# Performance work log

Hardware: AMD Instinct MI355X
Metric: run time of the kernel (lower is better)

## Reference

```python
import jax, jax.numpy as jnp
import numpy as np

B, N, H = 1024, 200, 64


def setup_inputs() -> dict:
    key = jax.random.key(0)
    ks = jax.random.split(key, 8)
    A = jax.random.uniform(ks[0], (B, 2 * N, N), dtype=jnp.float32)
    hidden = jax.random.normal(ks[1], (B, N, H), dtype=jnp.float32)
    s = 1.0 / np.sqrt(H)
    w_ih = jax.random.normal(ks[2], (3 * H, 2 * H), dtype=jnp.float32) * s
    w_hh = jax.random.normal(ks[3], (3 * H, H), dtype=jnp.float32) * s
    b_ih = jnp.zeros((3 * H,), jnp.float32)
    b_hh = jnp.zeros((3 * H,), jnp.float32)
    b_iah = jnp.zeros((H,), jnp.float32)
    b_oah = jnp.zeros((H,), jnp.float32)
    W_in = jax.random.normal(ks[4], (H, H), dtype=jnp.float32) * s
    bias_in = jnp.zeros((H,), jnp.float32)
    W_out = jax.random.normal(ks[5], (H, H), dtype=jnp.float32) * s
    bias_out = jnp.zeros((H,), jnp.float32)
    return {"A": A, "hidden": hidden, "w_ih": w_ih, "w_hh": w_hh,
            "b_ih": b_ih, "b_hh": b_hh, "b_iah": b_iah, "b_oah": b_oah,
            "W_in": W_in, "bias_in": bias_in, "W_out": W_out, "bias_out": bias_out}


def reference(A, hidden, w_ih, w_hh, b_ih, b_hh, b_iah, b_oah,
              W_in, bias_in, W_out, bias_out):
    # SessionGNN._cell, step=1.
    n = A.shape[1] // 2
    A_in, A_out = A[:, :n, :], A[:, n:, :]          # (B, N, N) each
    h_in = jnp.einsum('bnh,gh->bng', hidden, W_in) + bias_in    # (B, N, H)
    h_out = jnp.einsum('bnh,gh->bng', hidden, W_out) + bias_out
    input_in = jnp.matmul(A_in, h_in) + b_iah       # (B, N, H)
    input_out = jnp.matmul(A_out, h_out) + b_oah
    inputs = jnp.concatenate([input_in, input_out], axis=2)     # (B, N, 2H)
    gi = jnp.einsum('bni,gi->bng', inputs, w_ih) + b_ih         # (B, N, 3H)
    gh = jnp.einsum('bnh,gh->bng', hidden, w_hh) + b_hh
    i_r, i_i, i_n = jnp.split(gi, 3, axis=2)
    h_r, h_i, h_n = jnp.split(gh, 3, axis=2)
    resetgate = jax.nn.sigmoid(i_r + h_r)
    inputgate = jax.nn.sigmoid(i_i + h_i)
    newgate = jnp.tanh(i_n + resetgate * h_n)
    return hidden - inputgate * (hidden - newgate)
```

## Files before the change

kernel.cpp:

```cpp
#include <hip/hip_runtime.h>

typedef _Float16 f16;
typedef __attribute__((ext_vector_type(4))) _Float16 f16x4;
typedef __attribute__((ext_vector_type(8))) _Float16 f16x8;
typedef __attribute__((ext_vector_type(4))) float f32x4;

#define MFMA16(a, b, c) __builtin_amdgcn_mfma_f32_16x16x32_f16((a), (b), (c), 0, 0, 0)

__device__ __forceinline__ f16x8 cvt8(float4 a, float4 b) {
    f16x8 r;
    r[0] = (f16)a.x; r[1] = (f16)a.y; r[2] = (f16)a.z; r[3] = (f16)a.w;
    r[4] = (f16)b.x; r[5] = (f16)b.y; r[6] = (f16)b.z; r[7] = (f16)b.w;
    return r;
}

__device__ __forceinline__ f16x8 zero8() {
    f16x8 z;
#pragma unroll
    for (int q = 0; q < 8; ++q) z[q] = (f16)0.0f;
    return z;
}

__global__ void prep_kernel(const float* __restrict__ w_ih, const float* __restrict__ w_hh,
                            const float* __restrict__ b_ih, const float* __restrict__ b_hh,
                            const float* __restrict__ b_iah, const float* __restrict__ b_oah,
                            const float* __restrict__ W_in, const float* __restrict__ bias_in,
                            const float* __restrict__ W_out, const float* __restrict__ bias_out,
                            f16* __restrict__ Wc, f16* __restrict__ Whh, f16* __restrict__ Wih,
                            float* __restrict__ cstA, float* __restrict__ cstB,
                            float* __restrict__ biasc) {
    const int gid = blockIdx.x * 256 + threadIdx.x;
    const int gstride = gridDim.x * 256;
    for (int i = gid; i < 8192; i += gstride)
        Wc[i] = (f16)(i < 4096 ? W_in[i] : W_out[i - 4096]);
    for (int i = gid; i < 12288; i += gstride) Whh[i] = (f16)w_hh[i];
    for (int i = gid; i < 24576; i += gstride) Wih[i] = (f16)w_ih[i];
    for (int job = gid; job < 768; job += gstride) {
        const int g = job >> 2, q = job & 3;
        float s = (q == 0) ? b_ih[g] : 0.0f;
        const float* wr = w_ih + g * 128 + q * 32;
        for (int i = 0; i < 32; ++i)
            s += wr[i] * ((q * 32 + i < 64) ? b_iah[q * 32 + i] : b_oah[q * 32 + i - 64]);
        atomicAdd(&cstA[g], s);
    }
    for (int g = gid; g < 192; g += gstride) cstB[g] = b_hh[g];
    for (int j = gid; j < 128; j += gstride) biasc[j] = (j < 64) ? bias_in[j] : bias_out[j - 64];
}

__global__ void zero_kernel(float* __restrict__ cstA) {
    if (threadIdx.x < 192) cstA[threadIdx.x] = 0.0f;
}

__global__ __launch_bounds__(512, 2) void gru_fused(
    const float* __restrict__ A, const float* __restrict__ hidden,
    const f16* __restrict__ Wc, const f16* __restrict__ Whh, const f16* __restrict__ Wih,
    const float* __restrict__ cstA, const float* __restrict__ cstB,
    const float* __restrict__ biasc, float* __restrict__ out) {
    extern __shared__ __align__(16) char lds_raw[];
    f16* hT  = (f16*)lds_raw;
    f16* hA  = (f16*)(lds_raw + 51200);
    f16* inp = (f16*)lds_raw;

    const int b = blockIdx.x;
    const float* Ab = A + (size_t)b * 80000;
    const float* hb = hidden + (size_t)b * 12800;
    float* ob = out + (size_t)b * 12800;

    const int tid = threadIdx.x;
    const int w   = tid >> 6;
    const int l   = tid & 63;
    const int l15 = l & 15;
    const int lg  = l >> 4;

    for (int mt = w; mt < 13; mt += 8) {
        const int m  = mt * 16 + l15;
        const int mc = m < 200 ? m : 199;
        const float* hrow = hb + mc * 64;
        float4 r0 = *(const float4*)(hrow + lg * 8);
        float4 r1 = *(const float4*)(hrow + lg * 8 + 4);
        float4 r2 = *(const float4*)(hrow + 32 + lg * 8);
        float4 r3 = *(const float4*)(hrow + 32 + lg * 8 + 4);
        f16x8 a0 = cvt8(r0, r1), a1 = cvt8(r2, r3);
        const int m0 = mt * 16 + lg * 4;
#pragma unroll
        for (int jt = 0; jt < 8; ++jt) {
            const int j = jt * 16 + l15;
            f32x4 acc = {0.f, 0.f, 0.f, 0.f};
            acc = MFMA16(a0, *(const f16x8*)(Wc + j * 64 + lg * 8), acc);
            acc = MFMA16(a1, *(const f16x8*)(Wc + j * 64 + 32 + lg * 8), acc);
            const float bc = biasc[j];
            if (m0 < 200) {
                f16x4 pk;
                pk[0] = (f16)(acc[0] + bc); pk[1] = (f16)(acc[1] + bc);
                pk[2] = (f16)(acc[2] + bc); pk[3] = (f16)(acc[3] + bc);
                *(f16x4*)(hT + j * 200 + m0) = pk;
            }
        }
    }
    __syncthreads();

    const int hf = w >> 2;
    const f16* hTp = hT + (w * 16 + l15) * 200;

    int s_h[4], s_row[4], s_unit[4]; bool s_act[4];
#pragma unroll
    for (int r = 0; r < 4; ++r) {
        const int idx = tid + r * 512;
        s_act[r] = idx < 1600;
        const int ic = s_act[r] ? idx : 0;
        s_h[r] = ic / 800;
        const int rem = ic % 800;
        s_row[r] = rem / 50; s_unit[r] = rem % 50;
    }

#define P2_LOADS(T, V)                                                            \
    {                                                                             \
        _Pragma("unroll")                                                         \
        for (int r = 0; r < 4; ++r) if (s_act[r]) {                               \
            const int n = (T) * 16 + s_row[r];                                    \
            const int nc = n < 200 ? n : 199;                                     \
            V[r] = *(const float4*)(Ab + (size_t)(s_h[r] * 200 + nc) * 200        \
                                    + s_unit[r] * 4);                             \
        }                                                                         \
    }
#define P2_WRITE(BUF, V)                                                          \
    {                                                                             \
        _Pragma("unroll")                                                         \
        for (int r = 0; r < 4; ++r) if (s_act[r]) {                               \
            const int idx = tid + r * 512;                                        \
            f16x4 pk;                                                             \
            pk[0] = (f16)V[r].x; pk[1] = (f16)V[r].y;                             \
            pk[2] = (f16)V[r].z; pk[3] = (f16)V[r].w;                             \
            *(f16x4*)(hA + (BUF) * 6400 + idx * 4) = pk;                          \
        }                                                                         \
    }

    f32x4 accC[13];
#pragma unroll
    for (int t = 0; t < 13; ++t) accC[t] = (f32x4){0.f, 0.f, 0.f, 0.f};

    float4 vA[4], vB[4];
    P2_LOADS(0, vA);
    P2_WRITE(0, vA);
    P2_LOADS(1, vB);
    __syncthreads();

#pragma unroll
    for (int t = 0; t < 13; ++t) {
        if (t + 2 <= 12) {
            if ((t & 1) == 0) { P2_LOADS(t + 2, vA); }
            else              { P2_LOADS(t + 2, vB); }
        }
        {
            const f16* hAp = hA + (t & 1) * 6400 + hf * 3200 + l15 * 200;
#pragma unroll
            for (int k0 = 0; k0 < 224; k0 += 32) {
                const int koff = (k0 == 192) ? 192 : k0 + lg * 8;
                f16x8 a;
                if (k0 == 192 && lg != 0) a = zero8();
                else                      a = *(const f16x8*)(hAp + koff);
                f16x8 bf = *(const f16x8*)(hTp + koff);
                accC[t] = MFMA16(a, bf, accC[t]);
            }
        }
        if (t + 1 <= 12) {
            if (((t + 1) & 1) == 0) { P2_WRITE(0, vA); }
            else                    { P2_WRITE(1, vB); }
        }
        __syncthreads();
    }
#undef P2_LOADS
#undef P2_WRITE

#pragma unroll
    for (int t = 0; t < 13; ++t) {
#pragma unroll
        for (int r = 0; r < 4; ++r) {
            const int n = t * 16 + lg * 4 + r;
            if (n < 200) inp[n * 136 + w * 16 + l15] = (f16)accC[t][r];
        }
    }
    __syncthreads();

    const int c   = w & 3;
    const int wm2 = w >> 2;
    const int hcol = c * 16 + l15;
    f16x8 Wf0[4], Wf1[4], Wf2[4];
#pragma unroll
    for (int k = 0; k < 4; ++k) {
        Wf0[k] = *(const f16x8*)(Wih + (hcol      ) * 128 + k * 32 + lg * 8);
        Wf1[k] = *(const f16x8*)(Wih + (64  + hcol) * 128 + k * 32 + lg * 8);
        Wf2[k] = *(const f16x8*)(Wih + (128 + hcol) * 128 + k * 32 + lg * 8);
    }
    f16x8 Hf0[2], Hf1[2], Hf2[2];
#pragma unroll
    for (int k = 0; k < 2; ++k) {
        Hf0[k] = *(const f16x8*)(Whh + (hcol      ) * 64 + k * 32 + lg * 8);
        Hf1[k] = *(const f16x8*)(Whh + (64  + hcol) * 64 + k * 32 + lg * 8);
        Hf2[k] = *(const f16x8*)(Whh + (128 + hcol) * 64 + k * 32 + lg * 8);
    }
    const float cAr = cstA[hcol], cAi = cstA[64 + hcol], cAn = cstA[128 + hcol];
    const float cBr = cstB[hcol], cBi = cstB[64 + hcol], cBn = cstB[128 + hcol];

    for (int t = wm2; t < 13; t += 2) {
        const int n  = t * 16 + l15;
        const int nc = n < 200 ? n : 199;
        f32x4 gir = {0.f,0.f,0.f,0.f}, gii = {0.f,0.f,0.f,0.f}, gin = {0.f,0.f,0.f,0.f};
        f32x4 ghr = {0.f,0.f,0.f,0.f}, ghi = {0.f,0.f,0.f,0.f}, ghn = {0.f,0.f,0.f,0.f};
#pragma unroll
        for (int k = 0; k < 2; ++k) {
            const int h = k * 32 + lg * 8;
            float4 r0 = *(const float4*)(hb + nc * 64 + h);
            float4 r1 = *(const float4*)(hb + nc * 64 + h + 4);
            f16x8 a = cvt8(r0, r1);
            ghr = MFMA16(a, Hf0[k], ghr);
            ghi = MFMA16(a, Hf1[k], ghi);
            ghn = MFMA16(a, Hf2[k], ghn);
        }
#pragma unroll
        for (int k = 0; k < 4; ++k) {
            f16x8 a = *(const f16x8*)(inp + nc * 136 + k * 32 + lg * 8);
            gir = MFMA16(a, Wf0[k], gir);
            gii = MFMA16(a, Wf1[k], gii);
            gin = MFMA16(a, Wf2[k], gin);
        }
#pragma unroll
        for (int r = 0; r < 4; ++r) {
            const int row = t * 16 + lg * 4 + r;
            if (row < 200) {
                const float hv = hb[row * 64 + hcol];
                const float xr = gir[r] + ghr[r] + cAr + cBr;
                const float xi = gii[r] + ghi[r] + cAi + cBi;
                const float rg = 1.0f / (1.0f + __expf(-xr));
                const float ig = 1.0f / (1.0f + __expf(-xi));
                const float xn = gin[r] + cAn + rg * (ghn[r] + cBn);
                const float e2 = __expf(2.0f * xn);
                const float ng = 1.0f - 2.0f / (e2 + 1.0f);
                ob[row * 64 + hcol] = hv + ig * (ng - hv);
            }
        }
    }
}

extern "C" void kernel_launch(void* const* d_in, const int* in_sizes, int n_in,
                              void* d_out, int out_size, void* d_ws, size_t ws_size,
                              hipStream_t stream) {
    const float* A        = (const float*)d_in[0];
    const float* hidden   = (const float*)d_in[1];
    const float* w_ih     = (const float*)d_in[2];
    const float* w_hh     = (const float*)d_in[3];
    const float* b_ih     = (const float*)d_in[4];
    const float* b_hh     = (const float*)d_in[5];
    const float* b_iah    = (const float*)d_in[6];
    const float* b_oah    = (const float*)d_in[7];
    const float* W_in     = (const float*)d_in[8];
    const float* bias_in  = (const float*)d_in[9];
    const float* W_out    = (const float*)d_in[10];
    const float* bias_out = (const float*)d_in[11];
    float* out = (float*)d_out;

    char* wsb = (char*)d_ws;
    f16* Wc      = (f16*)wsb;
    f16* Whh     = Wc + 8192;
    f16* Wih     = Whh + 12288;
    float* cstA  = (float*)(wsb + 90112);
    float* cstB  = cstA + 192;
    float* biasc = cstB + 192;

    static const int kLds = 76800;
    hipFuncSetAttribute(reinterpret_cast<const void*>(gru_fused),
                        hipFuncAttributeMaxDynamicSharedMemorySize, kLds);

    zero_kernel<<<dim3(1), dim3(256), 0, stream>>>(cstA);
    prep_kernel<<<dim3(64), dim3(256), 0, stream>>>(
        w_ih, w_hh, b_ih, b_hh, b_iah, b_oah, W_in, bias_in, W_out, bias_out,
        Wc, Whh, Wih, cstA, cstB, biasc);
    gru_fused<<<dim3(1024), dim3(512), kLds, stream>>>(
        A, hidden, Wc, Whh, Wih, cstA, cstB, biasc, out);
}
```

Before: 153.0 us.

## Split adjacency contraction into two K-halves to shrink LDS and raise occupancy

```diff
diff --git a/kernel.cpp b/kernel.cpp
--- a/kernel.cpp
+++ b/kernel.cpp
@@ -14,11 +14,10 @@
     return r;
 }
 
-__device__ __forceinline__ f16x8 zero8() {
-    f16x8 z;
-#pragma unroll
-    for (int q = 0; q < 8; ++q) z[q] = (f16)0.0f;
-    return z;
+__device__ __forceinline__ f16x4 cvt4(float4 v) {
+    f16x4 r;
+    r[0] = (f16)v.x; r[1] = (f16)v.y; r[2] = (f16)v.z; r[3] = (f16)v.w;
+    return r;
 }
 
 __global__ void prep_kernel(const float* __restrict__ w_ih, const float* __restrict__ w_hh,
@@ -51,15 +50,15 @@
     if (threadIdx.x < 192) cstA[threadIdx.x] = 0.0f;
 }
 
-__global__ __launch_bounds__(512, 2) void gru_fused(
+__global__ __launch_bounds__(512, 3) void gru_fused(
     const float* __restrict__ A, const float* __restrict__ hidden,
     const f16* __restrict__ Wc, const f16* __restrict__ Whh, const f16* __restrict__ Wih,
     const float* __restrict__ cstA, const float* __restrict__ cstB,
     const float* __restrict__ biasc, float* __restrict__ out) {
-    extern __shared__ __align__(16) char lds_raw[];
-    f16* hT  = (f16*)lds_raw;
-    f16* hA  = (f16*)(lds_raw + 51200);
-    f16* inp = (f16*)lds_raw;
+    __shared__ __align__(16) char lds_raw[52224];
+    f16* hTc = (f16*)lds_raw;
+    f16* hA  = (f16*)(lds_raw + 34816);
+    char* inpB = lds_raw;
 
     const int b = blockIdx.x;
     const float* Ab = A + (size_t)b * 80000;
@@ -72,66 +71,47 @@
     const int l15 = l & 15;
     const int lg  = l >> 4;
 
-    for (int mt = w; mt < 13; mt += 8) {
-        const int m  = mt * 16 + l15;
-        const int mc = m < 200 ? m : 199;
-        const float* hrow = hb + mc * 64;
-        float4 r0 = *(const float4*)(hrow + lg * 8);
-        float4 r1 = *(const float4*)(hrow + lg * 8 + 4);
-        float4 r2 = *(const float4*)(hrow + 32 + lg * 8);
-        float4 r3 = *(const float4*)(hrow + 32 + lg * 8 + 4);
-        f16x8 a0 = cvt8(r0, r1), a1 = cvt8(r2, r3);
-        const int m0 = mt * 16 + lg * 4;
-#pragma unroll
-        for (int jt = 0; jt < 8; ++jt) {
-            const int j = jt * 16 + l15;
-            f32x4 acc = {0.f, 0.f, 0.f, 0.f};
-            acc = MFMA16(a0, *(const f16x8*)(Wc + j * 64 + lg * 8), acc);
-            acc = MFMA16(a1, *(const f16x8*)(Wc + j * 64 + 32 + lg * 8), acc);
-            const float bc = biasc[j];
-            if (m0 < 200) {
-                f16x4 pk;
-                pk[0] = (f16)(acc[0] + bc); pk[1] = (f16)(acc[1] + bc);
-                pk[2] = (f16)(acc[2] + bc); pk[3] = (f16)(acc[3] + bc);
-                *(f16x4*)(hT + j * 200 + m0) = pk;
-            }
-        }
-    }
-    __syncthreads();
-
+    for (int idx = tid; idx < 128 * 24; idx += 512) {
+        const int j = idx / 24, k = idx % 24;
+        hTc[j * 136 + 112 + k] = (f16)0.0f;
+    }
+    for (int idx = tid; idx < 2 * 2 * 16 * 36; idx += 512) {
+        const int bu = idx / 1152, rem = idx % 1152;
+        const int hh = rem / 576, rem2 = rem % 576;
+        const int rr = rem2 / 36, kk = rem2 % 36;
+        hA[bu * 4352 + hh * 2176 + rr * 136 + 100 + kk] = (f16)0.0f;
+    }
+
+    const f16* hTp = hTc + (w * 16 + l15) * 136;
     const int hf = w >> 2;
-    const f16* hTp = hT + (w * 16 + l15) * 200;
-
-    int s_h[4], s_row[4], s_unit[4]; bool s_act[4];
-#pragma unroll
-    for (int r = 0; r < 4; ++r) {
-        const int idx = tid + r * 512;
-        s_act[r] = idx < 1600;
-        const int ic = s_act[r] ? idx : 0;
-        s_h[r] = ic / 800;
-        const int rem = ic % 800;
-        s_row[r] = rem / 50; s_unit[r] = rem % 50;
-    }
-
-#define P2_LOADS(T, V)                                                            \
+
+    int s_h[2], s_row[2], s_unit[2]; bool s_act[2];
+#pragma unroll
+    for (int r = 0; r < 2; ++r) {
+        const int u = tid + r * 512;
+        s_act[r] = u < 800;
+        const int uc = s_act[r] ? u : 0;
+        s_h[r] = uc / 400;
+        const int rem = uc % 400;
+        s_row[r] = rem / 25; s_unit[r] = rem % 25;
+    }
+
+#define P2_LOADS(T, CO, V)                                                        \
     {                                                                             \
         _Pragma("unroll")                                                         \
-        for (int r = 0; r < 4; ++r) if (s_act[r]) {                               \
+        for (int r = 0; r < 2; ++r) if (s_act[r]) {                               \
             const int n = (T) * 16 + s_row[r];                                    \
             const int nc = n < 200 ? n : 199;                                     \
             V[r] = *(const float4*)(Ab + (size_t)(s_h[r] * 200 + nc) * 200        \
-                                    + s_unit[r] * 4);                             \
+                                    + (CO) + s_unit[r] * 4);                      \
         }                                                                         \
     }
 #define P2_WRITE(BUF, V)                                                          \
     {                                                                             \
         _Pragma("unroll")                                                         \
-        for (int r = 0; r < 4; ++r) if (s_act[r]) {                               \
-            const int idx = tid + r * 512;                                        \
-            f16x4 pk;                                                             \
-            pk[0] = (f16)V[r].x; pk[1] = (f16)V[r].y;                             \
-            pk[2] = (f16)V[r].z; pk[3] = (f16)V[r].w;                             \
-            *(f16x4*)(hA + (BUF) * 6400 + idx * 4) = pk;                          \
+        for (int r = 0; r < 2; ++r) if (s_act[r]) {                               \
+            *(f16x4*)(hA + (BUF) * 4352 + s_h[r] * 2176 + s_row[r] * 136          \
+                      + s_unit[r] * 4) = cvt4(V[r]);                              \
         }                                                                         \
     }
 
@@ -139,52 +119,89 @@
 #pragma unroll
     for (int t = 0; t < 13; ++t) accC[t] = (f32x4){0.f, 0.f, 0.f, 0.f};
 
-    float4 vA[4], vB[4];
-    P2_LOADS(0, vA);
-    P2_WRITE(0, vA);
-    P2_LOADS(1, vB);
-    __syncthreads();
-
-#pragma unroll
-    for (int t = 0; t < 13; ++t) {
-        if (t + 2 <= 12) {
-            if ((t & 1) == 0) { P2_LOADS(t + 2, vA); }
-            else              { P2_LOADS(t + 2, vB); }
-        }
-        {
-            const f16* hAp = hA + (t & 1) * 6400 + hf * 3200 + l15 * 200;
-#pragma unroll
-            for (int k0 = 0; k0 < 224; k0 += 32) {
-                const int koff = (k0 == 192) ? 192 : k0 + lg * 8;
-                f16x8 a;
-                if (k0 == 192 && lg != 0) a = zero8();
-                else                      a = *(const f16x8*)(hAp + koff);
-                f16x8 bf = *(const f16x8*)(hTp + koff);
-                accC[t] = MFMA16(a, bf, accC[t]);
-            }
-        }
-        if (t + 1 <= 12) {
-            if (((t + 1) & 1) == 0) { P2_WRITE(0, vA); }
-            else                    { P2_WRITE(1, vB); }
+    float4 vA[2], vB[2];
+
+    for (int c = 0; c < 2; ++c) {
+        const int cOff = c * 100;
+
+        if (w < 7) {
+            const int ml = w * 16 + l15;
+            const int mg = cOff + (ml < 100 ? ml : 99);
+            const float* hrow = hb + mg * 64;
+            float4 r0 = *(const float4*)(hrow + lg * 8);
+            float4 r1 = *(const float4*)(hrow + lg * 8 + 4);
+            float4 r2 = *(const float4*)(hrow + 32 + lg * 8);
+            float4 r3 = *(const float4*)(hrow + 32 + lg * 8 + 4);
+            f16x8 a0 = cvt8(r0, r1), a1 = cvt8(r2, r3);
+            const int m0 = w * 16 + lg * 4;
+            const bool valid = (m0 <= 96);
+#pragma unroll
+            for (int jt = 0; jt < 8; ++jt) {
+                const int j = jt * 16 + l15;
+                f32x4 acc = {0.f, 0.f, 0.f, 0.f};
+                acc = MFMA16(a0, *(const f16x8*)(Wc + j * 64 + lg * 8), acc);
+                acc = MFMA16(a1, *(const f16x8*)(Wc + j * 64 + 32 + lg * 8), acc);
+                const float bc = biasc[j];
+                f16x4 pk;
+                if (valid) {
+                    pk[0] = (f16)(acc[0] + bc); pk[1] = (f16)(acc[1] + bc);
+                    pk[2] = (f16)(acc[2] + bc); pk[3] = (f16)(acc[3] + bc);
+                } else {
+                    pk[0] = (f16)0.f; pk[1] = (f16)0.f; pk[2] = (f16)0.f; pk[3] = (f16)0.f;
+                }
+                *(f16x4*)(hTc + j * 136 + m0) = pk;
+            }
         }
         __syncthreads();
+
+        P2_LOADS(0, cOff, vA);
+        P2_WRITE(0, vA);
+        P2_LOADS(1, cOff, vB);
+        __syncthreads();
+
+#pragma unroll
+        for (int t = 0; t < 13; ++t) {
+            if (t + 2 <= 12) {
+                if ((t & 1) == 0) { P2_LOADS(t + 2, cOff, vA); }
+                else              { P2_LOADS(t + 2, cOff, vB); }
+            }
+            {
+                const f16* hAp = hA + (t & 1) * 4352 + hf * 2176 + l15 * 136;
+#pragma unroll
+                for (int k0 = 0; k0 < 128; k0 += 32) {
+                    const int koff = k0 + lg * 8;
+                    f16x8 a  = *(const f16x8*)(hAp + koff);
+                    f16x8 bf = *(const f16x8*)(hTp + koff);
+                    accC[t] = MFMA16(a, bf, accC[t]);
+                }
+            }
+            if (t + 1 <= 12) {
+                if (((t + 1) & 1) == 0) { P2_WRITE(0, vA); }
+                else                    { P2_WRITE(1, vB); }
+            }
+            __syncthreads();
+        }
     }
 #undef P2_LOADS
 #undef P2_WRITE
 
-#pragma unroll
-    for (int t = 0; t < 13; ++t) {
-#pragma unroll
-        for (int r = 0; r < 4; ++r) {
-            const int n = t * 16 + lg * 4 + r;
-            if (n < 200) inp[n * 136 + w * 16 + l15] = (f16)accC[t][r];
+    {
+        const int colb = (w * 16 + l15) * 2;
+#pragma unroll
+        for (int t = 0; t < 13; ++t) {
+#pragma unroll
+            for (int r = 0; r < 4; ++r) {
+                const int n = t * 16 + lg * 4 + r;
+                if (n < 200)
+                    *(f16*)(inpB + n * 256 + (colb ^ ((n & 7) << 4))) = (f16)accC[t][r];
+            }
         }
     }
     __syncthreads();
 
-    const int c   = w & 3;
-    const int wm2 = w >> 2;
-    const int hcol = c * 16 + l15;
+    const int c3   = w & 3;
+    const int wm2  = w >> 2;
+    const int hcol = c3 * 16 + l15;
     f16x8 Wf0[4], Wf1[4], Wf2[4];
 #pragma unroll
     for (int k = 0; k < 4; ++k) {
@@ -219,7 +236,8 @@
         }
 #pragma unroll
         for (int k = 0; k < 4; ++k) {
-            f16x8 a = *(const f16x8*)(inp + nc * 136 + k * 32 + lg * 8);
+            f16x8 a = *(const f16x8*)(inpB + nc * 256
+                                      + ((k * 64 + lg * 16) ^ ((nc & 7) << 4)));
             gir = MFMA16(a, Wf0[k], gir);
             gii = MFMA16(a, Wf1[k], gii);
             gin = MFMA16(a, Wf2[k], gin);
@@ -267,14 +285,10 @@
     float* cstB  = cstA + 192;
     float* biasc = cstB + 192;
 
-    static const int kLds = 76800;
-    hipFuncSetAttribute(reinterpret_cast<const void*>(gru_fused),
-                        hipFuncAttributeMaxDynamicSharedMemorySize, kLds);
-
     zero_kernel<<<dim3(1), dim3(256), 0, stream>>>(cstA);
     prep_kernel<<<dim3(64), dim3(256), 0, stream>>>(
         w_ih, w_hh, b_ih, b_hh, b_iah, b_oah, W_in, bias_in, W_out, bias_out,
         Wc, Whh, Wih, cstA, cstB, biasc);
-    gru_fused<<<dim3(1024), dim3(512), kLds, stream>>>(
+    gru_fused<<<dim3(1024), dim3(512), 0, stream>>>(
         A, hidden, Wc, Whh, Wih, cstA, cstB, biasc, out);
 }
```

Result: slower. 266.5 us (+74.2%).
